# Performance work log

Measured on AMD Instinct MI355X. Metric: run time of the kernel, lower is better.

Reference implementation:

```python
import jax, jax.numpy as jnp
import numpy as np

B, N, C_IN, C_H, C_OUT, R, X_DIM = 32, 256, 64, 128, 128, 5, 1024
NEG = -9e15

def _leaky(x, s=0.2):
    return jnp.where(x >= 0, x, s * x)

def gat_layer(atoms, mask, W, b, a):
    # atoms: (B,n,c_in), mask: (B,n,n,R) bool, W: (c_in, R*c), b: (R*c,), a: (R, 2c)
    bs, n, _ = atoms.shape
    c = a.shape[1] // 2
    h = (atoms @ W + b).reshape(bs, n, R, c)            # (B,n,R,c)
    src = jnp.einsum('bnrc,rc->bnr', h, a[:, :c])       # a . h_i part
    dst = jnp.einsum('bnrc,rc->bnr', h, a[:, c:])       # a . h_j part
    logits = _leaky(src[:, :, None, :] + dst[:, None, :, :])  # (B,i,j,R)
    masked = jnp.where(mask, logits, NEG)
    probs = jax.nn.softmax(masked.reshape(bs, n, n * R), axis=2).reshape(bs, n, n, R)
    return jnp.einsum('bijr,bjrc->bic', probs, h)       # (B,n,c)

def setup_inputs() -> dict:
    key = jax.random.key(0)
    ks = jax.random.split(key, 16)
    def p(k, shape, fan):
        return jax.random.normal(k, shape, jnp.float32) * (1.414 / np.sqrt(fan))
    inp = {
        'x': jax.random.normal(ks[0], (B, X_DIM), jnp.float32),
        'y_atoms': jax.random.normal(ks[1], (B, N, C_IN), jnp.float32),
        'y_bonds': jax.random.randint(ks[2], (B, N, N, R), 0, 2, jnp.int32),
        'W1': p(ks[3], (C_IN, R * C_H), C_IN), 'b1': jnp.zeros((R * C_H,), jnp.float32),
        'a1': p(ks[4], (R, 2 * C_H), 2 * C_H),
        'W2': p(ks[5], (C_H, R * C_H), C_H), 'b2': jnp.zeros((R * C_H,), jnp.float32),
        'a2': p(ks[6], (R, 2 * C_H), 2 * C_H),
        'W3': p(ks[7], (C_H, R * C_OUT), C_H), 'b3': jnp.zeros((R * C_OUT,), jnp.float32),
        'a3': p(ks[8], (R, 2 * C_OUT), 2 * C_OUT),
        'We1': p(ks[9], (2 * C_OUT + X_DIM, 256), 2 * C_OUT + X_DIM), 'be1': jnp.zeros((256,), jnp.float32),
        'We2': p(ks[10], (256, 32), 256), 'be2': jnp.zeros((32,), jnp.float32),
        'We3': p(ks[11], (32, 1), 32), 'be3': jnp.zeros((1,), jnp.float32),
    }
    return inp

def reference(x, y_atoms, y_bonds, W1, b1, a1, W2, b2, a2, W3, b3, a3,
              We1, be1, We2, be2, We3, be3):
    mask = (y_bonds == 1)
    h = gat_layer(y_atoms, mask, W1, b1, a1)
    h = _leaky(h)                                   # dropout is identity at eval
    h = gat_layer(h, mask, W2, b2, a2)
    h = _leaky(h)
    h = gat_layer(h, mask, W3, b3, a3)
    y_feats = jnp.concatenate([jnp.mean(h, axis=1), jnp.max(h, axis=1)], axis=1)
    z = jnp.concatenate([x, y_feats], axis=1)
    z = _leaky(z @ We1 + be1)
    z = _leaky(z @ We2 + be2)
    return z @ We3 + be3
```

## Files before the change

### kernel.cpp

```cpp
#include <hip/hip_runtime.h>
#include <cstddef>

#define NBLK 512

typedef __attribute__((ext_vector_type(8))) short bf16x8;
typedef __attribute__((ext_vector_type(4))) float f32x4;

__device__ __forceinline__ float lrelu(float x) { return x >= 0.f ? x : 0.2f * x; }
__device__ __forceinline__ unsigned short f2bf(float x) {
    unsigned u = __float_as_uint(x);
    u += 0x7FFFu + ((u >> 16) & 1u);
    return (unsigned short)(u >> 16);
}
__device__ __forceinline__ float bf2f(unsigned short u) {
    return __uint_as_float((unsigned)u << 16);
}

#define SY_CNT 0
#define SY_GA  256
#define SY_GR  512
#define SY_XB  1024
#define SY_XR  3072

__device__ __forceinline__ void xbar(unsigned* sync, int xcd, int r, unsigned cnt,
                                     unsigned ph, int t) {
    __syncthreads();
    if (t == 0) {
        __hip_atomic_fetch_add(&sync[SY_XB + (xcd * 8 + (r & 7)) * 32], 1u,
                               __ATOMIC_RELAXED, __HIP_MEMORY_SCOPE_AGENT);
        if (r == 0) {
            const unsigned tgt = cnt * ph;
            unsigned s;
            do {
                __builtin_amdgcn_s_sleep(1);
                s = 0;
#pragma unroll
                for (int i = 0; i < 8; ++i)
                    s += __hip_atomic_load(&sync[SY_XB + (xcd * 8 + i) * 32],
                                           __ATOMIC_RELAXED, __HIP_MEMORY_SCOPE_AGENT);
            } while (s < tgt);
#pragma unroll
            for (int g = 0; g < 4; ++g)
                __hip_atomic_store(&sync[SY_XR + (xcd * 4 + g) * 32], ph,
                                   __ATOMIC_RELAXED, __HIP_MEMORY_SCOPE_AGENT);
        } else {
            unsigned* w = &sync[SY_XR + (xcd * 4 + (r & 3)) * 32];
            while (__hip_atomic_load(w, __ATOMIC_RELAXED, __HIP_MEMORY_SCOPE_AGENT) < ph)
                __builtin_amdgcn_s_sleep(8);
        }
    }
    __syncthreads();
}

__device__ __forceinline__ void wtrans(const float* __restrict__ W,
                                       unsigned short* __restrict__ WT,
                                       int K, int nt, int t) {
    int n = nt * 64 + (t & 63);
    for (int kg = t >> 6; kg < K / 8; kg += 8) {
        bf16x8 v;
#pragma unroll
        for (int e = 0; e < 8; ++e) v[e] = (short)f2bf(W[(size_t)(kg * 8 + e) * 640 + n]);
        *(bf16x8*)&WT[(size_t)n * K + kg * 8] = v;
    }
}

__device__ __forceinline__ void maskpack(const int* __restrict__ bonds,
                                         unsigned char* __restrict__ maskp, int gt) {
    const int4* p = (const int4*)(bonds + (size_t)gt * 20);
    int4 q0 = p[0], q1 = p[1], q2 = p[2], q3 = p[3], q4 = p[4];
    int v[20] = {q0.x, q0.y, q0.z, q0.w, q1.x, q1.y, q1.z, q1.w,
                 q2.x, q2.y, q2.z, q2.w, q3.x, q3.y, q3.z, q3.w,
                 q4.x, q4.y, q4.z, q4.w};
    unsigned m = 0;
#pragma unroll
    for (int k = 0; k < 4; ++k)
#pragma unroll
        for (int r = 0; r < 5; ++r)
            m |= (v[k * 5 + r] == 1) ? (1u << (k * 8 + r)) : 0u;
    *(unsigned*)&maskp[(size_t)gt * 4] = m;
}

template <int K, int MODE>
__device__ __forceinline__ void gemm_body(int mt, int nt, int t,
                                          const float* __restrict__ Af32,
                                          const unsigned short* __restrict__ Ab,
                                          const unsigned short* __restrict__ WTg,
                                          const float* __restrict__ bias,
                                          const float* __restrict__ avec,
                                          float* __restrict__ srcp,
                                          float* __restrict__ dstp,
                                          unsigned short* __restrict__ hTf) {
    const int n0 = nt * 64, m0 = mt * 64;
    const int w = t >> 6, lane = t & 63;
    const int colg = lane & 15, rquad = lane >> 4;
    const int m = m0 + w * 16 + colg;
    const int koff = rquad * 8;

    bf16x8 afr[K / 32];
#pragma unroll
    for (int kk = 0; kk < K; kk += 32) {
        size_t off = (size_t)m * K + kk + koff;
        if (MODE == 1) {
            afr[kk >> 5] = *(const bf16x8*)&Ab[off];
        } else {
            float4 q0 = *(const float4*)&Af32[off];
            float4 q1 = *(const float4*)&Af32[off + 4];
            bf16x8 af;
            af[0] = (short)f2bf(q0.x); af[1] = (short)f2bf(q0.y);
            af[2] = (short)f2bf(q0.z); af[3] = (short)f2bf(q0.w);
            af[4] = (short)f2bf(q1.x); af[5] = (short)f2bf(q1.y);
            af[6] = (short)f2bf(q1.z); af[7] = (short)f2bf(q1.w);
            afr[kk >> 5] = af;
        }
    }
    f32x4 acc[4] = {};
#pragma unroll
    for (int kk = 0; kk < K; kk += 32) {
        bf16x8 af = afr[kk >> 5];
        bf16x8 b0 = *(const bf16x8*)&WTg[(size_t)(n0 + 0 * 16 + colg) * K + kk + koff];
        bf16x8 b1 = *(const bf16x8*)&WTg[(size_t)(n0 + 1 * 16 + colg) * K + kk + koff];
        bf16x8 b2 = *(const bf16x8*)&WTg[(size_t)(n0 + 2 * 16 + colg) * K + kk + koff];
        bf16x8 b3 = *(const bf16x8*)&WTg[(size_t)(n0 + 3 * 16 + colg) * K + kk + koff];
        acc[0] = __builtin_amdgcn_mfma_f32_16x16x32_bf16(af, b0, acc[0], 0, 0, 0);
        acc[1] = __builtin_amdgcn_mfma_f32_16x16x32_bf16(af, b1, acc[1], 0, 0, 0);
        acc[2] = __builtin_amdgcn_mfma_f32_16x16x32_bf16(af, b2, acc[2], 0, 0, 0);
        acc[3] = __builtin_amdgcn_mfma_f32_16x16x32_bf16(af, b3, acc[3], 0, 0, 0);
    }

    const int r = n0 >> 7, chalf = n0 & 127;
    const int b = m0 >> 8, jb = m0 & 255;
    float val[4][4];
    float ssum[4] = {0.f, 0.f, 0.f, 0.f}, dsum[4] = {0.f, 0.f, 0.f, 0.f};
#pragma unroll
    for (int ct = 0; ct < 4; ++ct) {
        int cg = chalf + ct * 16 + colg;
        float bv = bias[n0 + ct * 16 + colg];
        float asr = avec[r * 256 + cg];
        float ads = avec[r * 256 + 128 + cg];
#pragma unroll
        for (int reg = 0; reg < 4; ++reg) {
            float v = acc[ct][reg] + bv;
            val[ct][reg] = v;
            ssum[reg] += v * asr;
            dsum[reg] += v * ads;
        }
    }
#pragma unroll
    for (int mk = 1; mk < 16; mk <<= 1)
#pragma unroll
        for (int reg = 0; reg < 4; ++reg) {
            ssum[reg] += __shfl_xor(ssum[reg], mk);
            dsum[reg] += __shfl_xor(dsum[reg], mk);
        }
    if (colg == 0) {
        int nhalf = (n0 >> 6) & 1;
#pragma unroll
        for (int reg = 0; reg < 4; ++reg) {
            int row = m0 + w * 16 + rquad * 4 + reg;
            srcp[nhalf * 40960 + row * 5 + r] = ssum[reg];
            dstp[nhalf * 40960 + row * 5 + r] = dsum[reg];
        }
    }
    {
        const int joct = (jb >> 3) + w * 2 + (rquad >> 1);
        const size_t tile = (size_t)((b * 5 + r) * 32 + joct) * 1024;
        const int sub = (rquad & 1) * 4;
#pragma unroll
        for (int ct = 0; ct < 4; ++ct) {
            int c = chalf + ct * 16 + colg;
            uint2 pk;
            pk.x = (unsigned)f2bf(val[ct][0]) | ((unsigned)f2bf(val[ct][1]) << 16);
            pk.y = (unsigned)f2bf(val[ct][2]) | ((unsigned)f2bf(val[ct][3]) << 16);
            *(uint2*)&hTf[tile + (size_t)c * 8 + sub] = pk;
        }
    }
}

template <int FINAL>
__device__ __forceinline__ void agg_body(int b, int itile, int t, unsigned char* SM,
                                         const unsigned short* __restrict__ hTf,
                                         const float* __restrict__ srcp,
                                         const float* __restrict__ dstp,
                                         const unsigned char* __restrict__ maskp,
                                         unsigned short* __restrict__ Ab,
                                         float* __restrict__ poolS,
                                         float* __restrict__ poolM) {
    unsigned short* Ps = (unsigned short*)SM;
    float* Ds2l = (float*)(SM + 40960);
    float* Ss   = (float*)(SM + 46080);
    float* Zw   = (float*)(SM + 46400);
    float* Zrow = (float*)(SM + 46912);

    const int ib = b * 256 + itile * 16;
    const int w = t >> 6, lane = t & 63;
    const int colg = lane & 15, rquad = lane >> 4;
    const int c = w * 16 + colg;
    const size_t bbase = (size_t)(b * 5) * 32 * 1024;

    if (t < 80) Ss[t] = srcp[(size_t)ib * 5 + t] + srcp[40960 + (size_t)ib * 5 + t];
    for (int idx = t; idx < 1280; idx += 512) {
        int jl = idx & 255, rr = idx >> 8;
        size_t o = (size_t)(b * 256 + jl) * 5 + rr;
        Ds2l[rr * 256 + jl] = dstp[o] + dstp[40960 + o];
    }
    bf16x8 pre[4];
#pragma unroll
    for (int s = 0; s < 4; ++s)
        pre[s] = *(const bf16x8*)&hTf[bbase + (size_t)(s * 4 + rquad) * 1024 + (size_t)c * 8];
    __syncthreads();

    {
        const int i = t & 15;
        const int kq = (t >> 4) & 3;
        uint2 mk[5];
#pragma unroll
        for (int it = 0; it < 5; ++it) {
            int p = it * 512 + t;
            int s = p >> 6;
            int k0 = s * 32 + kq * 8;
            mk[it] = *(const uint2*)&maskp[((size_t)(ib + i) << 8) + (k0 & 255)];
        }
        float esum = 0.f;
#pragma unroll
        for (int it = 0; it < 5; ++it) {
            int p = it * 512 + t;
            int s = p >> 6;
            int k0 = s * 32 + kq * 8;
            int rr = k0 >> 8, j0 = k0 & 255;
            uint2 mk8 = mk[it];
            float sv = Ss[i * 5 + rr];
            float4 d0 = *(const float4*)&Ds2l[rr * 256 + j0];
            float4 d1 = *(const float4*)&Ds2l[rr * 256 + j0 + 4];
            float dv[8] = {d0.x, d0.y, d0.z, d0.w, d1.x, d1.y, d1.z, d1.w};
            bf16x8 pv;
#pragma unroll
            for (int e = 0; e < 8; ++e) {
                unsigned mb = ((e < 4 ? (mk8.x >> (8 * e)) : (mk8.y >> (8 * (e - 4)))) >> rr) & 1u;
                float vv = lrelu(sv + dv[e]);
                float ev = mb ? __expf(vv) : 0.f;
                unsigned short q = f2bf(ev);
                pv[e] = (short)q;
                esum += __uint_as_float((unsigned)q << 16);
            }
            *(bf16x8*)&Ps[p * 8] = pv;
        }
        esum += __shfl_xor(esum, 16);
        esum += __shfl_xor(esum, 32);
        if (lane < 16) Zw[w * 16 + (lane & 15)] = esum;
    }
    __syncthreads();
    if (t < 16) {
        float z = 0.f;
#pragma unroll
        for (int ww = 0; ww < 8; ++ww) z += Zw[ww * 16 + t];
        Zrow[t] = 1.f / z;
    }

    f32x4 acc0 = {}, acc1 = {};
#pragma unroll
    for (int s = 0; s < 4; ++s) {
        bf16x8 af = *(const bf16x8*)&Ps[(s * 64 + lane) * 8];
        if (s & 1) acc1 = __builtin_amdgcn_mfma_f32_16x16x32_bf16(af, pre[s], acc1, 0, 0, 0);
        else       acc0 = __builtin_amdgcn_mfma_f32_16x16x32_bf16(af, pre[s], acc0, 0, 0, 0);
    }
    {
        bf16x8 aq[4], bq[4];
#pragma unroll
        for (int q = 0; q < 4; ++q) {
            int s = 4 + q;
            aq[q] = *(const bf16x8*)&Ps[(s * 64 + lane) * 8];
            bq[q] = *(const bf16x8*)&hTf[bbase +
                (size_t)((s >> 3) * 32 + (s & 7) * 4 + rquad) * 1024 + (size_t)c * 8];
        }
#pragma unroll
        for (int q = 0; q < 4; ++q) {
            if (q & 1) acc1 = __builtin_amdgcn_mfma_f32_16x16x32_bf16(aq[q], bq[q], acc1, 0, 0, 0);
            else       acc0 = __builtin_amdgcn_mfma_f32_16x16x32_bf16(aq[q], bq[q], acc0, 0, 0, 0);
        }
    }
    for (int s8 = 8; s8 < 40; s8 += 8) {
        bf16x8 aq[8], bq[8];
#pragma unroll
        for (int q = 0; q < 8; ++q) {
            int s = s8 + q;
            aq[q] = *(const bf16x8*)&Ps[(s * 64 + lane) * 8];
            bq[q] = *(const bf16x8*)&hTf[bbase +
                (size_t)((s >> 3) * 32 + (s & 7) * 4 + rquad) * 1024 + (size_t)c * 8];
        }
#pragma unroll
        for (int q = 0; q < 8; ++q) {
            if (q & 1) acc1 = __builtin_amdgcn_mfma_f32_16x16x32_bf16(aq[q], bq[q], acc1, 0, 0, 0);
            else       acc0 = __builtin_amdgcn_mfma_f32_16x16x32_bf16(aq[q], bq[q], acc0, 0, 0, 0);
        }
    }
    __syncthreads();
    const int irow = ib + rquad * 4;
    if (FINAL) {
        float ps = 0.f, pm = -3.4e38f;
#pragma unroll
        for (int reg = 0; reg < 4; ++reg) {
            float v = (acc0[reg] + acc1[reg]) * Zrow[rquad * 4 + reg];
            ps += v;
            pm = fmaxf(pm, v);
        }
        ps += __shfl_xor(ps, 16);
        ps += __shfl_xor(ps, 32);
        pm = fmaxf(pm, __shfl_xor(pm, 16));
        pm = fmaxf(pm, __shfl_xor(pm, 32));
        if (rquad == 0) {
            poolS[(size_t)(b * 16 + itile) * 128 + c] = ps;
            poolM[(size_t)(b * 16 + itile) * 128 + c] = pm;
        }
    } else {
#pragma unroll
        for (int reg = 0; reg < 4; ++reg) {
            float v = (acc0[reg] + acc1[reg]) * Zrow[rquad * 4 + reg];
            Ab[(size_t)(irow + reg) * 128 + c] = f2bf(lrelu(v));
        }
    }
}

__device__ __forceinline__ void mlp_fused(int b, int t, unsigned char* SM,
                                          const float* __restrict__ x,
                                          const float* __restrict__ poolS,
                                          const float* __restrict__ poolM,
                                          const float* __restrict__ We1,
                                          const float* __restrict__ be1,
                                          const float* __restrict__ We2,
                                          const float* __restrict__ be2,
                                          const float* __restrict__ We3,
                                          const float* __restrict__ be3,
                                          float* __restrict__ out) {
    float* zs  = (float*)SM;
    float* p16 = (float*)(SM + 5120);
    float* z1s = (float*)(SM + 37888);
    float* s2p = (float*)(SM + 38912);
    float* z2s = (float*)(SM + 39936);
    __syncthreads();
    for (int k = t; k < 1280; k += 512) {
        float v;
        if (k < 1024) {
            v = x[(size_t)b * 1024 + k];
        } else if (k < 1152) {
            int f = k - 1024;
            float s = 0.f;
#pragma unroll
            for (int it = 0; it < 16; ++it) s += poolS[(size_t)(b * 16 + it) * 128 + f];
            v = s * (1.f / 256.f);
        } else {
            int f = k - 1152;
            float mx = -3.4e38f;
#pragma unroll
            for (int it = 0; it < 16; ++it) mx = fmaxf(mx, poolM[(size_t)(b * 16 + it) * 128 + f]);
            v = mx;
        }
        zs[k] = v;
    }
    __syncthreads();
    const int o = t & 255, half = t >> 8;
#pragma unroll
    for (int kc = 0; kc < 16; ++kc) {
        float s = 0.f;
#pragma unroll 8
        for (int kk = 0; kk < 40; ++kk)
            s += zs[kc * 80 + half * 40 + kk] * We1[(size_t)(kc * 80 + half * 40 + kk) * 256 + o];
        p16[kc * 512 + half * 256 + o] = s;
    }
    __syncthreads();
    if (t < 256) {
        float s = be1[t];
#pragma unroll
        for (int kc = 0; kc < 16; ++kc)
            s += p16[kc * 512 + t] + p16[kc * 512 + 256 + t];
        z1s[t] = lrelu(s);
    }
    __syncthreads();
    if (t < 256) {
        int oo = t & 31, g = t >> 5;
        float p = 0.f;
#pragma unroll
        for (int k = 0; k < 32; ++k) p += z1s[g * 32 + k] * We2[(g * 32 + k) * 32 + oo];
        s2p[g * 32 + oo] = p;
    }
    __syncthreads();
    if (t < 32) {
        float s2 = be2[t];
#pragma unroll
        for (int g = 0; g < 8; ++g) s2 += s2p[g * 32 + t];
        z2s[t] = lrelu(s2);
    }
    __syncthreads();
    if (t == 0) {
        float s3 = be3[0];
#pragma unroll
        for (int k = 0; k < 32; ++k) s3 += z2s[k] * We3[k];
        out[b] = s3;
    }
}

constexpr size_t O_MASK  = 0;
constexpr size_t O_SRC   = 2097152;  constexpr size_t SRC_SZ = 327680;
constexpr size_t O_DST   = O_SRC + 3 * SRC_SZ;
constexpr size_t O_AB    = O_DST + 3 * SRC_SZ;  constexpr size_t AB_SZ = 2097152;
constexpr size_t O_HT    = O_AB + 2 * AB_SZ;    constexpr size_t HT_SZ = 10485760;
constexpr size_t O_WTX   = O_HT + 3 * HT_SZ;    constexpr size_t WTX_SZ = 409600;
constexpr size_t O_POOLS = O_WTX + 8 * WTX_SZ;
constexpr size_t O_POOLM = O_POOLS + 262144;
constexpr size_t O_SYNC  = O_POOLM + 262144;

__global__ __launch_bounds__(512, 4) void k_mega(
    const float* __restrict__ x, const float* __restrict__ y_atoms,
    const int* __restrict__ bonds,
    const float* __restrict__ W1, const float* __restrict__ b1, const float* __restrict__ a1,
    const float* __restrict__ W2, const float* __restrict__ b2, const float* __restrict__ a2,
    const float* __restrict__ W3, const float* __restrict__ b3, const float* __restrict__ a3,
    const float* __restrict__ We1, const float* __restrict__ be1,
    const float* __restrict__ We2, const float* __restrict__ be2,
    const float* __restrict__ We3, const float* __restrict__ be3,
    char* __restrict__ ws, float* __restrict__ out) {
    __shared__ __align__(16) unsigned char SM[46976];
    __shared__ unsigned s_nfo[3];
    const int rb = blockIdx.x;
    const int t = threadIdx.x;
    const int hb = t >> 8, t2 = t & 255;

    unsigned char* maskp = (unsigned char*)(ws + O_MASK);
    unsigned* sync = (unsigned*)(ws + O_SYNC);
    float* poolS = (float*)(ws + O_POOLS);
    float* poolM = (float*)(ws + O_POOLM);

    if (t == 0) {
        unsigned xr;
        asm volatile("s_getreg_b32 %0, hwreg(HW_REG_XCC_ID)" : "=s"(xr));
        xr &= 7u;
        unsigned rk = __hip_atomic_fetch_add(&sync[SY_CNT + xr * 32], 1u,
                                             __ATOMIC_RELAXED, __HIP_MEMORY_SCOPE_AGENT);
        s_nfo[0] = xr;
        s_nfo[1] = rk;
    }
    __syncthreads();
    const int xcd = (int)s_nfo[0];
    const int r0 = (int)s_nfo[1];

    unsigned short* WT1x = (unsigned short*)(ws + O_WTX + (size_t)xcd * WTX_SZ);
    unsigned short* WT2x = WT1x + 40960;
    unsigned short* WT3x = WT2x + 81920;

    if (r0 < 10)      wtrans(W1, WT1x, 64, r0, t);
    else if (r0 < 20) wtrans(W2, WT2x, 128, r0 - 10, t);
    else if (r0 < 30) wtrans(W3, WT3x, 128, r0 - 20, t);
    for (unsigned u = (unsigned)r0 * 512u + t; u < 65536u; u += 64u * 512u) {
        int b = xcd + (int)(u >> 14) * 8;
        maskpack(bonds, maskp, b * 16384 + (int)(u & 16383u));
    }
    __syncthreads();

    if (t == 0) {
        __hip_atomic_fetch_add(&sync[SY_GA + (rb & 7) * 32], 1u,
                               __ATOMIC_RELAXED, __HIP_MEMORY_SCOPE_AGENT);
        if (rb == 0) {
            unsigned s;
            do {
                __builtin_amdgcn_s_sleep(1);
                s = 0;
#pragma unroll
                for (int i = 0; i < 8; ++i)
                    s += __hip_atomic_load(&sync[SY_GA + i * 32],
                                           __ATOMIC_RELAXED, __HIP_MEMORY_SCOPE_AGENT);
            } while (s < NBLK);
#pragma unroll
            for (int g = 0; g < 16; ++g)
                __hip_atomic_store(&sync[SY_GR + g * 32], 1u,
                                   __ATOMIC_RELAXED, __HIP_MEMORY_SCOPE_AGENT);
        } else {
            unsigned* w = &sync[SY_GR + (rb >> 5) * 32];
            while (__hip_atomic_load(w, __ATOMIC_RELAXED, __HIP_MEMORY_SCOPE_AGENT) < 1u)
                __builtin_amdgcn_s_sleep(8);
        }
        s_nfo[2] = __hip_atomic_load(&sync[SY_CNT + xcd * 32],
                                     __ATOMIC_RELAXED, __HIP_MEMORY_SCOPE_AGENT);
    }
    __syncthreads();
    const unsigned cnt = s_nfo[2];

    float* src0 = (float*)(ws + O_SRC);
    float* src1 = (float*)(ws + O_SRC + SRC_SZ);
    float* src2 = (float*)(ws + O_SRC + 2 * SRC_SZ);
    float* dst0 = (float*)(ws + O_DST);
    float* dst1 = (float*)(ws + O_DST + SRC_SZ);
    float* dst2 = (float*)(ws + O_DST + 2 * SRC_SZ);
    unsigned short* Ab0 = (unsigned short*)(ws + O_AB);
    unsigned short* Ab1 = (unsigned short*)(ws + O_AB + AB_SZ);
    unsigned short* hT0 = (unsigned short*)(ws + O_HT);
    unsigned short* hT1 = (unsigned short*)(ws + O_HT + HT_SZ);
    unsigned short* hT2 = (unsigned short*)(ws + O_HT + 2 * HT_SZ);

    if (cnt != 64u) {
        for (int u = 0; u < 10; ++u) wtrans(W1, WT1x, 64, u, t);
        for (int u = 0; u < 10; ++u) wtrans(W2, WT2x, 128, u, t);
        for (int u = 0; u < 10; ++u) wtrans(W3, WT3x, 128, u, t);
        __syncthreads();
        for (unsigned u = t; u < 65536u; u += 512u) {
            int b = xcd + (int)(u >> 14) * 8;
            maskpack(bonds, maskp, b * 16384 + (int)(u & 16383u));
        }
    }
    for (int u = 2 * r0 + hb; u < 160; u += 2 * (int)cnt) {
        int b = xcd + (u & 3) * 8;
        int mt = b * 4 + ((u >> 2) & 3), nt = u >> 4;
        gemm_body<64, 0>(mt, nt, t2, y_atoms, nullptr, WT1x, b1, a1, src0, dst0, hT0);
    }
    xbar(sync, xcd, r0, cnt, 1, t);

    for (int u = r0; u < 64; u += (int)cnt)
        agg_body<0>(xcd + (u & 3) * 8, u >> 2, t, SM, hT0, src0, dst0, maskp,
                    Ab0, nullptr, nullptr);
    xbar(sync, xcd, r0, cnt, 2, t);

    for (int u = 2 * r0 + hb; u < 160; u += 2 * (int)cnt) {
        int b = xcd + (u & 3) * 8;
        int mt = b * 4 + ((u >> 2) & 3), nt = u >> 4;
        gemm_body<128, 1>(mt, nt, t2, nullptr, Ab0, WT2x, b2, a2, src1, dst1, hT1);
    }
    xbar(sync, xcd, r0, cnt, 3, t);

    for (int u = r0; u < 64; u += (int)cnt)
        agg_body<0>(xcd + (u & 3) * 8, u >> 2, t, SM, hT1, src1, dst1, maskp,
                    Ab1, nullptr, nullptr);
    xbar(sync, xcd, r0, cnt, 4, t);

    for (int u = 2 * r0 + hb; u < 160; u += 2 * (int)cnt) {
        int b = xcd + (u & 3) * 8;
        int mt = b * 4 + ((u >> 2) & 3), nt = u >> 4;
        gemm_body<128, 1>(mt, nt, t2, nullptr, Ab1, WT3x, b3, a3, src2, dst2, hT2);
    }
    xbar(sync, xcd, r0, cnt, 5, t);

    for (int u = r0; u < 64; u += (int)cnt)
        agg_body<1>(xcd + (u & 3) * 8, u >> 2, t, SM, hT2, src2, dst2, maskp,
                    nullptr, poolS, poolM);
    xbar(sync, xcd, r0, cnt, 6, t);

    for (int u = r0; u < 4; u += (int)cnt)
        mlp_fused(xcd + u * 8, t, SM, x, poolS, poolM, We1, be1, We2, be2, We3, be3, out);
}

extern "C" void kernel_launch(void* const* d_in, const int* in_sizes, int n_in,
                              void* d_out, int out_size, void* d_ws, size_t ws_size,
                              hipStream_t stream) {
    const float* x       = (const float*)d_in[0];
    const float* y_atoms = (const float*)d_in[1];
    const int*   y_bonds = (const int*)d_in[2];
    const float* W1 = (const float*)d_in[3];
    const float* b1 = (const float*)d_in[4];
    const float* a1 = (const float*)d_in[5];
    const float* W2 = (const float*)d_in[6];
    const float* b2 = (const float*)d_in[7];
    const float* a2 = (const float*)d_in[8];
    const float* W3 = (const float*)d_in[9];
    const float* b3 = (const float*)d_in[10];
    const float* a3 = (const float*)d_in[11];
    const float* We1 = (const float*)d_in[12];
    const float* be1 = (const float*)d_in[13];
    const float* We2 = (const float*)d_in[14];
    const float* be2 = (const float*)d_in[15];
    const float* We3 = (const float*)d_in[16];
    const float* be3 = (const float*)d_in[17];
    float* out = (float*)d_out;
    char* ws = (char*)d_ws;

    hipMemsetAsync(ws + O_SYNC, 0, 16384, stream);
    k_mega<<<NBLK, 512, 0, stream>>>(
        x, y_atoms, y_bonds, W1, b1, a1, W2, b2, a2, W3, b3, a3,
        We1, be1, We2, be2, We3, be3, ws, out);
}
```

Measured before the change: 244.2 us.

## Double block size to 1024 threads and split aggregation K across wave halves

Raises the persistent megakernel's block from 512 to 1024 threads. Each phase is re-partitioned for this: GEMM tiles go to four quarter-blocks, the aggregation splits its 40 K-steps between two groups of 8 waves with an LDS reduction, and the MLP and mask packing loops are re-strided. Register prefetching in the GEMM and aggregation is dropped to make room for the doubled wave count under launch_bounds(1024,8). This risks register spills and an extra LDS reduction and barrier in exchange for more waves hiding latency.

```diff
diff --git a/kernel.cpp b/kernel.cpp
--- a/kernel.cpp
+++ b/kernel.cpp
@@ -56,7 +56,7 @@
                                        unsigned short* __restrict__ WT,
                                        int K, int nt, int t) {
     int n = nt * 64 + (t & 63);
-    for (int kg = t >> 6; kg < K / 8; kg += 8) {
+    for (int kg = t >> 6; kg < K / 8; kg += 16) {
         bf16x8 v;
 #pragma unroll
         for (int e = 0; e < 8; ++e) v[e] = (short)f2bf(W[(size_t)(kg * 8 + e) * 640 + n]);
@@ -96,35 +96,26 @@
     const int m = m0 + w * 16 + colg;
     const int koff = rquad * 8;
 
-    bf16x8 afr[K / 32];
+    f32x4 acc[4] = {};
 #pragma unroll
     for (int kk = 0; kk < K; kk += 32) {
+        bf16x8 af;
         size_t off = (size_t)m * K + kk + koff;
         if (MODE == 1) {
-            afr[kk >> 5] = *(const bf16x8*)&Ab[off];
+            af = *(const bf16x8*)&Ab[off];
         } else {
             float4 q0 = *(const float4*)&Af32[off];
             float4 q1 = *(const float4*)&Af32[off + 4];
-            bf16x8 af;
             af[0] = (short)f2bf(q0.x); af[1] = (short)f2bf(q0.y);
             af[2] = (short)f2bf(q0.z); af[3] = (short)f2bf(q0.w);
             af[4] = (short)f2bf(q1.x); af[5] = (short)f2bf(q1.y);
             af[6] = (short)f2bf(q1.z); af[7] = (short)f2bf(q1.w);
-            afr[kk >> 5] = af;
-        }
-    }
-    f32x4 acc[4] = {};
-#pragma unroll
-    for (int kk = 0; kk < K; kk += 32) {
-        bf16x8 af = afr[kk >> 5];
-        bf16x8 b0 = *(const bf16x8*)&WTg[(size_t)(n0 + 0 * 16 + colg) * K + kk + koff];
-        bf16x8 b1 = *(const bf16x8*)&WTg[(size_t)(n0 + 1 * 16 + colg) * K + kk + koff];
-        bf16x8 b2 = *(const bf16x8*)&WTg[(size_t)(n0 + 2 * 16 + colg) * K + kk + koff];
-        bf16x8 b3 = *(const bf16x8*)&WTg[(size_t)(n0 + 3 * 16 + colg) * K + kk + koff];
-        acc[0] = __builtin_amdgcn_mfma_f32_16x16x32_bf16(af, b0, acc[0], 0, 0, 0);
-        acc[1] = __builtin_amdgcn_mfma_f32_16x16x32_bf16(af, b1, acc[1], 0, 0, 0);
-        acc[2] = __builtin_amdgcn_mfma_f32_16x16x32_bf16(af, b2, acc[2], 0, 0, 0);
-        acc[3] = __builtin_amdgcn_mfma_f32_16x16x32_bf16(af, b3, acc[3], 0, 0, 0);
+        }
+#pragma unroll
+        for (int ct = 0; ct < 4; ++ct) {
+            bf16x8 bfv = *(const bf16x8*)&WTg[(size_t)(n0 + ct * 16 + colg) * K + kk + koff];
+            acc[ct] = __builtin_amdgcn_mfma_f32_16x16x32_bf16(af, bfv, acc[ct], 0, 0, 0);
+        }
     }
 
     const int r = n0 >> 7, chalf = n0 & 127;
@@ -186,63 +177,53 @@
                                          float* __restrict__ poolS,
                                          float* __restrict__ poolM) {
     unsigned short* Ps = (unsigned short*)SM;
+    float* accb = (float*)SM;
     float* Ds2l = (float*)(SM + 40960);
     float* Ss   = (float*)(SM + 46080);
     float* Zw   = (float*)(SM + 46400);
-    float* Zrow = (float*)(SM + 46912);
+    float* Zrow = (float*)(SM + 47424);
 
     const int ib = b * 256 + itile * 16;
     const int w = t >> 6, lane = t & 63;
     const int colg = lane & 15, rquad = lane >> 4;
-    const int c = w * 16 + colg;
     const size_t bbase = (size_t)(b * 5) * 32 * 1024;
 
     if (t < 80) Ss[t] = srcp[(size_t)ib * 5 + t] + srcp[40960 + (size_t)ib * 5 + t];
-    for (int idx = t; idx < 1280; idx += 512) {
+    for (int idx = t; idx < 1280; idx += 1024) {
         int jl = idx & 255, rr = idx >> 8;
         size_t o = (size_t)(b * 256 + jl) * 5 + rr;
         Ds2l[rr * 256 + jl] = dstp[o] + dstp[40960 + o];
     }
-    bf16x8 pre[4];
-#pragma unroll
-    for (int s = 0; s < 4; ++s)
-        pre[s] = *(const bf16x8*)&hTf[bbase + (size_t)(s * 4 + rquad) * 1024 + (size_t)c * 8];
     __syncthreads();
 
     {
         const int i = t & 15;
         const int kq = (t >> 4) & 3;
-        uint2 mk[5];
-#pragma unroll
-        for (int it = 0; it < 5; ++it) {
-            int p = it * 512 + t;
-            int s = p >> 6;
-            int k0 = s * 32 + kq * 8;
-            mk[it] = *(const uint2*)&maskp[((size_t)(ib + i) << 8) + (k0 & 255)];
-        }
         float esum = 0.f;
 #pragma unroll
-        for (int it = 0; it < 5; ++it) {
-            int p = it * 512 + t;
-            int s = p >> 6;
-            int k0 = s * 32 + kq * 8;
-            int rr = k0 >> 8, j0 = k0 & 255;
-            uint2 mk8 = mk[it];
-            float sv = Ss[i * 5 + rr];
-            float4 d0 = *(const float4*)&Ds2l[rr * 256 + j0];
-            float4 d1 = *(const float4*)&Ds2l[rr * 256 + j0 + 4];
-            float dv[8] = {d0.x, d0.y, d0.z, d0.w, d1.x, d1.y, d1.z, d1.w};
-            bf16x8 pv;
-#pragma unroll
-            for (int e = 0; e < 8; ++e) {
-                unsigned mb = ((e < 4 ? (mk8.x >> (8 * e)) : (mk8.y >> (8 * (e - 4)))) >> rr) & 1u;
-                float vv = lrelu(sv + dv[e]);
-                float ev = mb ? __expf(vv) : 0.f;
-                unsigned short q = f2bf(ev);
-                pv[e] = (short)q;
-                esum += __uint_as_float((unsigned)q << 16);
+        for (int it = 0; it < 3; ++it) {
+            int p = it * 1024 + t;
+            if (p < 2560) {
+                int s = p >> 6;
+                int k0 = s * 32 + kq * 8;
+                int rr = k0 >> 8, j0 = k0 & 255;
+                uint2 mk8 = *(const uint2*)&maskp[((size_t)(ib + i) << 8) + j0];
+                float sv = Ss[i * 5 + rr];
+                float4 d0 = *(const float4*)&Ds2l[rr * 256 + j0];
+                float4 d1 = *(const float4*)&Ds2l[rr * 256 + j0 + 4];
+                float dv[8] = {d0.x, d0.y, d0.z, d0.w, d1.x, d1.y, d1.z, d1.w};
+                bf16x8 pv;
+#pragma unroll
+                for (int e = 0; e < 8; ++e) {
+                    unsigned mb = ((e < 4 ? (mk8.x >> (8 * e)) : (mk8.y >> (8 * (e - 4)))) >> rr) & 1u;
+                    float vv = lrelu(sv + dv[e]);
+                    float ev = mb ? __expf(vv) : 0.f;
+                    unsigned short q = f2bf(ev);
+                    pv[e] = (short)q;
+                    esum += __uint_as_float((unsigned)q << 16);
+                }
+                *(bf16x8*)&Ps[p * 8] = pv;
             }
-            *(bf16x8*)&Ps[p * 8] = pv;
         }
         esum += __shfl_xor(esum, 16);
         esum += __shfl_xor(esum, 32);
@@ -252,70 +233,56 @@
     if (t < 16) {
         float z = 0.f;
 #pragma unroll
-        for (int ww = 0; ww < 8; ++ww) z += Zw[ww * 16 + t];
+        for (int ww = 0; ww < 16; ++ww) z += Zw[ww * 16 + t];
         Zrow[t] = 1.f / z;
     }
 
+    const int c = (w & 7) * 16 + colg;
+    const int sbase = (w >> 3) * 20;
     f32x4 acc0 = {}, acc1 = {};
-#pragma unroll
-    for (int s = 0; s < 4; ++s) {
+#pragma unroll 4
+    for (int q = 0; q < 20; ++q) {
+        int s = sbase + q;
         bf16x8 af = *(const bf16x8*)&Ps[(s * 64 + lane) * 8];
-        if (s & 1) acc1 = __builtin_amdgcn_mfma_f32_16x16x32_bf16(af, pre[s], acc1, 0, 0, 0);
-        else       acc0 = __builtin_amdgcn_mfma_f32_16x16x32_bf16(af, pre[s], acc0, 0, 0, 0);
-    }
+        bf16x8 bfv = *(const bf16x8*)&hTf[bbase +
+            (size_t)((s >> 3) * 32 + (s & 7) * 4 + rquad) * 1024 + (size_t)c * 8];
+        if (q & 1) acc1 = __builtin_amdgcn_mfma_f32_16x16x32_bf16(af, bfv, acc1, 0, 0, 0);
+        else       acc0 = __builtin_amdgcn_mfma_f32_16x16x32_bf16(af, bfv, acc0, 0, 0, 0);
+    }
+    __syncthreads();
     {
-        bf16x8 aq[4], bq[4];
-#pragma unroll
-        for (int q = 0; q < 4; ++q) {
-            int s = 4 + q;
-            aq[q] = *(const bf16x8*)&Ps[(s * 64 + lane) * 8];
-            bq[q] = *(const bf16x8*)&hTf[bbase +
-                (size_t)((s >> 3) * 32 + (s & 7) * 4 + rquad) * 1024 + (size_t)c * 8];
-        }
-#pragma unroll
-        for (int q = 0; q < 4; ++q) {
-            if (q & 1) acc1 = __builtin_amdgcn_mfma_f32_16x16x32_bf16(aq[q], bq[q], acc1, 0, 0, 0);
-            else       acc0 = __builtin_amdgcn_mfma_f32_16x16x32_bf16(aq[q], bq[q], acc0, 0, 0, 0);
-        }
-    }
-    for (int s8 = 8; s8 < 40; s8 += 8) {
-        bf16x8 aq[8], bq[8];
-#pragma unroll
-        for (int q = 0; q < 8; ++q) {
-            int s = s8 + q;
-            aq[q] = *(const bf16x8*)&Ps[(s * 64 + lane) * 8];
-            bq[q] = *(const bf16x8*)&hTf[bbase +
-                (size_t)((s >> 3) * 32 + (s & 7) * 4 + rquad) * 1024 + (size_t)c * 8];
-        }
-#pragma unroll
-        for (int q = 0; q < 8; ++q) {
-            if (q & 1) acc1 = __builtin_amdgcn_mfma_f32_16x16x32_bf16(aq[q], bq[q], acc1, 0, 0, 0);
-            else       acc0 = __builtin_amdgcn_mfma_f32_16x16x32_bf16(aq[q], bq[q], acc0, 0, 0, 0);
-        }
-    }
-    __syncthreads();
-    const int irow = ib + rquad * 4;
-    if (FINAL) {
-        float ps = 0.f, pm = -3.4e38f;
-#pragma unroll
-        for (int reg = 0; reg < 4; ++reg) {
-            float v = (acc0[reg] + acc1[reg]) * Zrow[rquad * 4 + reg];
-            ps += v;
-            pm = fmaxf(pm, v);
-        }
-        ps += __shfl_xor(ps, 16);
-        ps += __shfl_xor(ps, 32);
-        pm = fmaxf(pm, __shfl_xor(pm, 16));
-        pm = fmaxf(pm, __shfl_xor(pm, 32));
-        if (rquad == 0) {
-            poolS[(size_t)(b * 16 + itile) * 128 + c] = ps;
-            poolM[(size_t)(b * 16 + itile) * 128 + c] = pm;
-        }
-    } else {
-#pragma unroll
-        for (int reg = 0; reg < 4; ++reg) {
-            float v = (acc0[reg] + acc1[reg]) * Zrow[rquad * 4 + reg];
-            Ab[(size_t)(irow + reg) * 128 + c] = f2bf(lrelu(v));
+        f32x4 ac;
+#pragma unroll
+        for (int reg = 0; reg < 4; ++reg) ac[reg] = acc0[reg] + acc1[reg];
+        *(f32x4*)&accb[(size_t)(w * 64 + lane) * 4] = ac;
+    }
+    __syncthreads();
+    if (t < 512) {
+        f32x4 pa = *(const f32x4*)&accb[(size_t)(w * 64 + lane) * 4];
+        f32x4 pb = *(const f32x4*)&accb[(size_t)((w + 8) * 64 + lane) * 4];
+        const int irow = ib + rquad * 4;
+        if (FINAL) {
+            float ps = 0.f, pm = -3.4e38f;
+#pragma unroll
+            for (int reg = 0; reg < 4; ++reg) {
+                float v = (pa[reg] + pb[reg]) * Zrow[rquad * 4 + reg];
+                ps += v;
+                pm = fmaxf(pm, v);
+            }
+            ps += __shfl_xor(ps, 16);
+            ps += __shfl_xor(ps, 32);
+            pm = fmaxf(pm, __shfl_xor(pm, 16));
+            pm = fmaxf(pm, __shfl_xor(pm, 32));
+            if (rquad == 0) {
+                poolS[(size_t)(b * 16 + itile) * 128 + c] = ps;
+                poolM[(size_t)(b * 16 + itile) * 128 + c] = pm;
+            }
+        } else {
+#pragma unroll
+            for (int reg = 0; reg < 4; ++reg) {
+                float v = (pa[reg] + pb[reg]) * Zrow[rquad * 4 + reg];
+                Ab[(size_t)(irow + reg) * 128 + c] = f2bf(lrelu(v));
+            }
         }
     }
 }
@@ -333,11 +300,11 @@
                                           float* __restrict__ out) {
     float* zs  = (float*)SM;
     float* p16 = (float*)(SM + 5120);
-    float* z1s = (float*)(SM + 37888);
-    float* s2p = (float*)(SM + 38912);
-    float* z2s = (float*)(SM + 39936);
-    __syncthreads();
-    for (int k = t; k < 1280; k += 512) {
+    float* z1s = (float*)(SM + 21504);
+    float* s2p = (float*)(SM + 22528);
+    float* z2s = (float*)(SM + 23552);
+    __syncthreads();
+    for (int k = t; k < 1280; k += 1024) {
         float v;
         if (k < 1024) {
             v = x[(size_t)b * 1024 + k];
@@ -357,21 +324,23 @@
         zs[k] = v;
     }
     __syncthreads();
-    const int o = t & 255, half = t >> 8;
-#pragma unroll
-    for (int kc = 0; kc < 16; ++kc) {
-        float s = 0.f;
+    {
+        const int o = t & 255, q4 = t >> 8;
+#pragma unroll
+        for (int j = 0; j < 4; ++j) {
+            int kc = q4 * 4 + j;
+            float s = 0.f;
 #pragma unroll 8
-        for (int kk = 0; kk < 40; ++kk)
-            s += zs[kc * 80 + half * 40 + kk] * We1[(size_t)(kc * 80 + half * 40 + kk) * 256 + o];
-        p16[kc * 512 + half * 256 + o] = s;
+            for (int kk = 0; kk < 80; ++kk)
+                s += zs[kc * 80 + kk] * We1[(size_t)(kc * 80 + kk) * 256 + o];
+            p16[kc * 256 + o] = s;
+        }
     }
     __syncthreads();
     if (t < 256) {
         float s = be1[t];
 #pragma unroll
-        for (int kc = 0; kc < 16; ++kc)
-            s += p16[kc * 512 + t] + p16[kc * 512 + 256 + t];
+        for (int kc = 0; kc < 16; ++kc) s += p16[kc * 256 + t];
         z1s[t] = lrelu(s);
     }
     __syncthreads();
@@ -408,7 +377,7 @@
 constexpr size_t O_POOLM = O_POOLS + 262144;
 constexpr size_t O_SYNC  = O_POOLM + 262144;
 
-__global__ __launch_bounds__(512, 4) void k_mega(
+__global__ __launch_bounds__(1024, 8) void k_mega(
     const float* __restrict__ x, const float* __restrict__ y_atoms,
     const int* __restrict__ bonds,
     const float* __restrict__ W1, const float* __restrict__ b1, const float* __restrict__ a1,
@@ -418,11 +387,11 @@
     const float* __restrict__ We2, const float* __restrict__ be2,
     const float* __restrict__ We3, const float* __restrict__ be3,
     char* __restrict__ ws, float* __restrict__ out) {
-    __shared__ __align__(16) unsigned char SM[46976];
+    __shared__ __align__(16) unsigned char SM[47488];
     __shared__ unsigned s_nfo[3];
     const int rb = blockIdx.x;
     const int t = threadIdx.x;
-    const int hb = t >> 8, t2 = t & 255;
+    const int q4 = t >> 8, t4 = t & 255;
 
     unsigned char* maskp = (unsigned char*)(ws + O_MASK);
     unsigned* sync = (unsigned*)(ws + O_SYNC);
@@ -449,9 +418,12 @@
     if (r0 < 10)      wtrans(W1, WT1x, 64, r0, t);
     else if (r0 < 20) wtrans(W2, WT2x, 128, r0 - 10, t);
     else if (r0 < 30) wtrans(W3, WT3x, 128, r0 - 20, t);
-    for (unsigned u = (unsigned)r0 * 512u + t; u < 65536u; u += 64u * 512u) {
-        int b = xcd + (int)(u >> 14) * 8;
-        maskpack(bonds, maskp, b * 16384 + (int)(u & 16383u));
+    {
+        unsigned u = (unsigned)r0 * 1024u + (unsigned)t;
+        if (u < 65536u) {
+            int b = xcd + (int)(u >> 14) * 8;
+            maskpack(bonds, maskp, b * 16384 + (int)(u & 16383u));
+        }
     }
     __syncthreads();
 
@@ -500,15 +472,15 @@
         for (int u = 0; u < 10; ++u) wtrans(W2, WT2x, 128, u, t);
         for (int u = 0; u < 10; ++u) wtrans(W3, WT3x, 128, u, t);
         __syncthreads();
-        for (unsigned u = t; u < 65536u; u += 512u) {
+        for (unsigned u = t; u < 65536u; u += 1024u) {
             int b = xcd + (int)(u >> 14) * 8;
             maskpack(bonds, maskp, b * 16384 + (int)(u & 16383u));
         }
     }
-    for (int u = 2 * r0 + hb; u < 160; u += 2 * (int)cnt) {
+    for (int u = (int)cnt * q4 + r0; u < 160; u += 4 * (int)cnt) {
         int b = xcd + (u & 3) * 8;
         int mt = b * 4 + ((u >> 2) & 3), nt = u >> 4;
-        gemm_body<64, 0>(mt, nt, t2, y_atoms, nullptr, WT1x, b1, a1, src0, dst0, hT0);
+        gemm_body<64, 0>(mt, nt, t4, y_atoms, nullptr, WT1x, b1, a1, src0, dst0, hT0);
     }
     xbar(sync, xcd, r0, cnt, 1, t);
 
@@ -517,10 +489,10 @@
                     Ab0, nullptr, nullptr);
     xbar(sync, xcd, r0, cnt, 2, t);
 
-    for (int u = 2 * r0 + hb; u < 160; u += 2 * (int)cnt) {
+    for (int u = (int)cnt * q4 + r0; u < 160; u += 4 * (int)cnt) {
         int b = xcd + (u & 3) * 8;
         int mt = b * 4 + ((u >> 2) & 3), nt = u >> 4;
-        gemm_body<128, 1>(mt, nt, t2, nullptr, Ab0, WT2x, b2, a2, src1, dst1, hT1);
+        gemm_body<128, 1>(mt, nt, t4, nullptr, Ab0, WT2x, b2, a2, src1, dst1, hT1);
     }
     xbar(sync, xcd, r0, cnt, 3, t);
 
@@ -529,10 +501,10 @@
                     Ab1, nullptr, nullptr);
     xbar(sync, xcd, r0, cnt, 4, t);
 
-    for (int u = 2 * r0 + hb; u < 160; u += 2 * (int)cnt) {
+    for (int u = (int)cnt * q4 + r0; u < 160; u += 4 * (int)cnt) {
         int b = xcd + (u & 3) * 8;
         int mt = b * 4 + ((u >> 2) & 3), nt = u >> 4;
-        gemm_body<128, 1>(mt, nt, t2, nullptr, Ab1, WT3x, b3, a3, src2, dst2, hT2);
+        gemm_body<128, 1>(mt, nt, t4, nullptr, Ab1, WT3x, b3, a3, src2, dst2, hT2);
     }
     xbar(sync, xcd, r0, cnt, 5, t);
 
@@ -570,7 +542,7 @@
     char* ws = (char*)d_ws;
 
     hipMemsetAsync(ws + O_SYNC, 0, 16384, stream);
-    k_mega<<<NBLK, 512, 0, stream>>>(
+    k_mega<<<NBLK, 1024, 0, stream>>>(
         x, y_atoms, y_bonds, W1, b1, a1, W2, b2, a2, W3, b3, a3,
         We1, be1, We2, be2, We3, be3, ws, out);
 }
```

New measurement: 358.4 us. 1.47x slower.
